# Kernel tuning notes

Measured on AMD Instinct MI355X. Metric: run time of the kernel, lower is better.

Reference implementation:

```python
import jax, jax.numpy as jnp
import numpy as np

N = 50000          # nodes
E = 1_600_000      # edges
DIN = 128          # input feature dim
HID = 32           # hidden_dim per head
HEADS = 4          # conv1 heads
G = 64             # graphs in batch
SLOPE = 0.2        # LeakyReLU negative slope (PyG GATConv default)
EPS = 1e-16


def setup_inputs() -> dict:
    key = jax.random.key(0)
    ks = jax.random.split(key, 14)
    s = 0.05
    return {
        "x": jax.random.normal(ks[0], (N, DIN), jnp.float32),
        "edge_index": jax.random.randint(ks[1], (2, E), 0, N, dtype=jnp.int64),
        "batch": jnp.sort(jax.random.randint(ks[2], (N,), 0, G, dtype=jnp.int64)),
        # conv1: GATConv(DIN, HID, heads=4, concat=True)
        "W1": jax.random.normal(ks[3], (DIN, HEADS * HID), jnp.float32) * s,
        "a_src1": jax.random.normal(ks[4], (HEADS, HID), jnp.float32) * s,
        "a_dst1": jax.random.normal(ks[5], (HEADS, HID), jnp.float32) * s,
        "b1": jax.random.normal(ks[6], (HEADS * HID,), jnp.float32) * s,
        # conv2: GATConv(4*HID, HID, heads=1)
        "W2": jax.random.normal(ks[7], (HEADS * HID, HID), jnp.float32) * s,
        "a_src2": jax.random.normal(ks[8], (1, HID), jnp.float32) * s,
        "a_dst2": jax.random.normal(ks[9], (1, HID), jnp.float32) * s,
        "b2": jax.random.normal(ks[10], (HID,), jnp.float32) * s,
        # final Linear(HID, 2)
        "Wfc": jax.random.normal(ks[11], (HID, 2), jnp.float32) * s,
        "bfc": jax.random.normal(ks[12], (2,), jnp.float32) * s,
    }


def gat_conv(x, src, dst, W, a_src, a_dst, b, heads, d):
    """PyG-style GATConv (self-loops already appended to src/dst)."""
    n = x.shape[0]
    h = (x @ W).reshape(n, heads, d)                   # [N,H,D]
    alpha_src = jnp.einsum('nhd,hd->nh', h, a_src)     # [N,H]
    alpha_dst = jnp.einsum('nhd,hd->nh', h, a_dst)     # [N,H]
    e = alpha_src[src] + alpha_dst[dst]                # [Etot,H]
    e = jnp.where(e >= 0, e, SLOPE * e)                # LeakyReLU
    # segment softmax over destination nodes
    m = jax.ops.segment_max(e, dst, num_segments=n)    # [N,H]
    e = jnp.exp(e - m[dst])
    s = jax.ops.segment_sum(e, dst, num_segments=n)    # [N,H]
    alpha = e / (s[dst] + EPS)                         # [Etot,H]
    msg = h[src] * alpha[:, :, None]                   # [Etot,H,D]
    out = jax.ops.segment_sum(msg, dst, num_segments=n)  # [N,H,D]
    return out.reshape(n, heads * d) + b               # concat heads + bias


def reference(x, edge_index, batch, W1, a_src1, a_dst1, b1,
              W2, a_src2, a_dst2, b2, Wfc, bfc):
    n = x.shape[0]
    loops = jnp.arange(n, dtype=edge_index.dtype)
    src = jnp.concatenate([edge_index[0], loops])      # add self loops
    dst = jnp.concatenate([edge_index[1], loops])

    h = gat_conv(x, src, dst, W1, a_src1, a_dst1, b1, HEADS, HID)
    h = jax.nn.elu(h)
    h = gat_conv(h, src, dst, W2, a_src2, a_dst2, b2, 1, HID)
    h = jax.nn.elu(h)

    # global mean pool over graphs
    sums = jax.ops.segment_sum(h, batch, num_segments=G)            # [G,HID]
    cnt = jax.ops.segment_sum(jnp.ones((n, 1), h.dtype), batch, num_segments=G)
    pooled = sums / jnp.maximum(cnt, 1.0)

    logits = pooled @ Wfc + bfc                                      # [G,2]
    return jax.nn.log_softmax(logits, axis=1)
```

## Files before the change

### kernel.cpp

```cpp
#include <hip/hip_runtime.h>
#include <hip/hip_fp8.h>
#include <math.h>

#define DIN   128
#define HEADS 4
#define HID   32
#define C1    (HEADS*HID)
#define NG    64
#define SLOPE 0.2f
#define EPSF  1e-16f

#define NPB   256
#define CAPQ  10240
#define CHUNK 2048

__device__ __forceinline__ unsigned int f2bf(float f) {
    unsigned int u = __float_as_uint(f);
    return (u + 0x7FFFu + ((u >> 16) & 1u)) >> 16;
}
__device__ __forceinline__ float bf_lo(unsigned int u) { return __uint_as_float(u << 16); }
__device__ __forceinline__ float bf_hi(unsigned int u) { return __uint_as_float(u & 0xFFFF0000u); }

__device__ __forceinline__ unsigned int f2fp8(float f) {
    __hip_fp8_e4m3 t(f);
    return (unsigned int)t.__x;
}
template <int SEL>
__device__ __forceinline__ float fp8tof(unsigned int u) {
#if __has_builtin(__builtin_amdgcn_cvt_f32_fp8)
    return __builtin_amdgcn_cvt_f32_fp8(u, SEL);
#else
    __hip_fp8_e4m3 t; t.__x = (unsigned char)((u >> (8 * SEL)) & 0xFFu); return (float)t;
#endif
}
typedef float f32x2 __attribute__((ext_vector_type(2)));
template <int WORD>
__device__ __forceinline__ f32x2 fp8pk(unsigned int u) {
#if __has_builtin(__builtin_amdgcn_cvt_pk_f32_fp8)
    return __builtin_amdgcn_cvt_pk_f32_fp8((int)u, WORD);
#else
    f32x2 r; r[0] = fp8tof<2 * WORD>(u); r[1] = fp8tof<2 * WORD + 1>(u); return r;
#endif
}

template <int NT>
__device__ __forceinline__ int blockScanExcl(int v, int* wsum) {
    int lane = threadIdx.x & 63, wid = threadIdx.x >> 6;
    int incl = v;
#pragma unroll
    for (int d = 1; d < 64; d <<= 1) {
        int t = __shfl_up(incl, d);
        if (lane >= d) incl += t;
    }
    if (lane == 63) wsum[wid] = incl;
    __syncthreads();
    if (threadIdx.x == 0) {
        int a = 0;
#pragma unroll
        for (int w = 0; w < NT / 64; w++) { int t = wsum[w]; wsum[w] = a; a += t; }
    }
    __syncthreads();
    return incl - v + wsum[wid];
}

__global__ void k_zero(int* gcursor, int nbuck) {
    int i = threadIdx.x;
    if (i < nbuck) gcursor[i] = 0;
}

__global__ __launch_bounds__(256) void k_binscatter(const int* __restrict__ srcs,
        const int* __restrict__ dsts, int* __restrict__ gcursor,
        unsigned int* __restrict__ stage, int E) {
    __shared__ unsigned int s_tmp[CHUNK];
    __shared__ unsigned int s_out[CHUNK];
    __shared__ int s_hist[256], s_off[256], s_base[256], s_cur[256], wsum[4];
    int tid = threadIdx.x;
    int e0 = blockIdx.x * CHUNK;
    int cnt = min(CHUNK, E - e0);
    s_hist[tid] = 0;
    __syncthreads();
    for (int i = tid; i < cnt; i += 256) {
        int sv = srcs[e0 + i];
        int dv = dsts[e0 + i];
        int b = dv >> 8;
        s_tmp[i] = ((unsigned)b << 24) | ((unsigned)(dv & (NPB - 1)) << 16) | (unsigned)sv;
        atomicAdd(&s_hist[b], 1);
    }
    __syncthreads();
    int myc = s_hist[tid];
    int excl = blockScanExcl<256>(myc, wsum);
    s_off[tid] = excl;
    s_base[tid] = myc ? atomicAdd(&gcursor[tid], myc) : 0;
    s_cur[tid] = 0;
    __syncthreads();
    for (int i = tid; i < cnt; i += 256) {
        unsigned int p = s_tmp[i];
        int b = p >> 24;
        int pos = s_off[b] + atomicAdd(&s_cur[b], 1);
        s_out[pos] = p;
    }
    __syncthreads();
    for (int i = tid; i < cnt; i += 256) {
        unsigned int p = s_out[i];
        int b = p >> 24;
        int rel = s_base[b] + (i - s_off[b]);
        if (rel < CAPQ) stage[(size_t)b * CAPQ + rel] = p & 0xFFFFFFu;
    }
}

__global__ __launch_bounds__(512) void k_bucket_build(const unsigned int* __restrict__ stage,
        const int* __restrict__ gcursor,
        int* __restrict__ rowstart, int* __restrict__ rowlen,
        int* __restrict__ esrc, int n) {
    __shared__ unsigned int s_e[CAPQ];
    __shared__ int s_cnt[256], s_offn[256], s_curn[256], wsum[8];
    __shared__ int s_eb;
    int bx = blockIdx.x, tid = threadIdx.x;
    int b = bx >> 1, hf = bx & 1;
    int cnt = min(gcursor[b], CAPQ);
    int node0 = b << 8;
    if (tid == 0) s_eb = 0;
    if (tid < 256) { s_cnt[tid] = 0; s_curn[tid] = 0; }
    __syncthreads();
    if (tid < b) atomicAdd(&s_eb, min(gcursor[tid], CAPQ));
    for (int i = tid; i < cnt; i += 512) {
        unsigned int p = stage[(size_t)b * CAPQ + i];
        s_e[i] = p;
        atomicAdd(&s_cnt[p >> 16], 1);
    }
    __syncthreads();
    int eb = s_eb;
    int myc = (tid < 256) ? s_cnt[tid] : 0;
    int excl = blockScanExcl<512>(myc, wsum);
    if (tid < 256) s_offn[tid] = excl;
    __syncthreads();
    if (tid < 128) {
        int ld = (hf << 7) + tid;
        int node = node0 + ld;
        if (node < n) { rowstart[node] = eb + s_offn[ld]; rowlen[node] = s_cnt[ld]; }
    }
    for (int i = tid; i < cnt; i += 512) {
        unsigned int p = s_e[i];
        int ld = p >> 16;
        if ((ld >> 7) == hf) {
            int pos = s_offn[ld] + atomicAdd(&s_curn[ld], 1);
            esrc[eb + pos] = (int)(p & 0xFFFFu);
        }
    }
}

#define BM1 64
#define BK1 32
__global__ __launch_bounds__(256) void k_conv1(const float* __restrict__ x, const float* __restrict__ W1,
                        const float* __restrict__ a_src, const float* __restrict__ a_dst,
                        unsigned char* __restrict__ h1f8, float* __restrict__ as1,
                        float* __restrict__ ad1, int n) {
    __shared__ float xt[BK1][BM1 + 1];
    __shared__ float ws[BK1][C1];
    int tid = threadIdx.x;
    int m0 = blockIdx.x * BM1;
    int ty = tid >> 4;
    int tx = tid & 15;
    int r0 = ty * 4;
    int c0 = tx * 8;
    float acc[4][8];
#pragma unroll
    for (int i = 0; i < 4; i++)
#pragma unroll
        for (int j = 0; j < 8; j++) acc[i][j] = 0.0f;

    for (int kb = 0; kb < DIN; kb += BK1) {
        {
            int row = tid >> 3;
            int c4  = (tid & 7) * 4;
#pragma unroll
            for (int i = 0; i < 2; i++) {
                int rr = row + i * 32;
                int g = m0 + rr;
                float4 v = make_float4(0.f, 0.f, 0.f, 0.f);
                if (g < n) v = *reinterpret_cast<const float4*>(x + (size_t)g * DIN + kb + c4);
                xt[c4 + 0][rr] = v.x; xt[c4 + 1][rr] = v.y;
                xt[c4 + 2][rr] = v.z; xt[c4 + 3][rr] = v.w;
            }
            int c4w = (tid & 31) * 4;
            int k0  = tid >> 5;
#pragma unroll
            for (int i = 0; i < 4; i++) {
                int kk = k0 + i * 8;
                *reinterpret_cast<float4*>(&ws[kk][c4w]) =
                    *reinterpret_cast<const float4*>(W1 + (size_t)(kb + kk) * C1 + c4w);
            }
        }
        __syncthreads();
#pragma unroll
        for (int kk = 0; kk < BK1; kk++) {
            float a[4], bb[8];
            *reinterpret_cast<float4*>(a)      = *reinterpret_cast<float4*>(&xt[kk][r0]);
            *reinterpret_cast<float4*>(bb)     = *reinterpret_cast<float4*>(&ws[kk][c0]);
            *reinterpret_cast<float4*>(bb + 4) = *reinterpret_cast<float4*>(&ws[kk][c0 + 4]);
#pragma unroll
            for (int i = 0; i < 4; i++)
#pragma unroll
                for (int j = 0; j < 8; j++) acc[i][j] = fmaf(a[i], bb[j], acc[i][j]);
        }
        __syncthreads();
    }
    float asv[8], adv[8];
#pragma unroll
    for (int j = 0; j < 8; j++) { asv[j] = a_src[c0 + j]; adv[j] = a_dst[c0 + j]; }
#pragma unroll
    for (int i = 0; i < 4; i++) {
        int g = m0 + r0 + i;
        float ps = 0.0f, pd = 0.0f;
#pragma unroll
        for (int j = 0; j < 8; j++) {
            ps = fmaf(acc[i][j], asv[j], ps);
            pd = fmaf(acc[i][j], adv[j], pd);
        }
        if (g < n) {
            unsigned int w0 = 0, w1 = 0;
#pragma unroll
            for (int j = 0; j < 4; j++) w0 |= f2fp8(acc[i][j]) << (8 * j);
#pragma unroll
            for (int j = 0; j < 4; j++) w1 |= f2fp8(acc[i][4 + j]) << (8 * j);
            *reinterpret_cast<uint2*>(h1f8 + (size_t)g * C1 + c0) = make_uint2(w0, w1);
        }
        ps += __shfl_xor(ps, 1); ps += __shfl_xor(ps, 2);
        pd += __shfl_xor(pd, 1); pd += __shfl_xor(pd, 2);
        if ((tx & 3) == 0 && g < n) {
            as1[g * HEADS + (tx >> 2)] = ps;
            ad1[g * HEADS + (tx >> 2)] = pd;
        }
    }
}

#define BM2 128
#define BK2 32
__global__ __launch_bounds__(256) void k_conv2(const unsigned int* __restrict__ x2u,
                        const float* __restrict__ W2,
                        const float* __restrict__ a_src, const float* __restrict__ a_dst,
                        unsigned char* __restrict__ h2f8, float* __restrict__ as2,
                        float* __restrict__ ad2, int n) {
    __shared__ float xt[BK2][BM2 + 1];
    __shared__ float ws[BK2][HID];
    int tid = threadIdx.x;
    int m0 = blockIdx.x * BM2;
    int ty = tid >> 3;
    int tx = tid & 7;
    int r0 = ty * 4;
    int c0 = tx * 4;
    float acc[4][4];
#pragma unroll
    for (int i = 0; i < 4; i++)
#pragma unroll
        for (int j = 0; j < 4; j++) acc[i][j] = 0.0f;

    for (int kb = 0; kb < C1; kb += BK2) {
        {
            int row = tid >> 3;
            int c4  = (tid & 7) * 4;
#pragma unroll
            for (int i = 0; i < 4; i++) {
                int rr = row + i * 32;
                int g = m0 + rr;
                uint2 u = make_uint2(0u, 0u);
                if (g < n) u = *reinterpret_cast<const uint2*>(x2u + (size_t)g * 64 + ((kb + c4) >> 1));
                xt[c4 + 0][rr] = bf_lo(u.x); xt[c4 + 1][rr] = bf_hi(u.x);
                xt[c4 + 2][rr] = bf_lo(u.y); xt[c4 + 3][rr] = bf_hi(u.y);
            }
            int kk = tid >> 3;
            int c4w = (tid & 7) * 4;
            *reinterpret_cast<float4*>(&ws[kk][c4w]) =
                *reinterpret_cast<const float4*>(W2 + (size_t)(kb + kk) * HID + c4w);
        }
        __syncthreads();
#pragma unroll
        for (int kk = 0; kk < BK2; kk++) {
            float a[4], bb[4];
            *reinterpret_cast<float4*>(a)  = *reinterpret_cast<float4*>(&xt[kk][r0]);
            *reinterpret_cast<float4*>(bb) = *reinterpret_cast<float4*>(&ws[kk][c0]);
#pragma unroll
            for (int i = 0; i < 4; i++)
#pragma unroll
                for (int j = 0; j < 4; j++) acc[i][j] = fmaf(a[i], bb[j], acc[i][j]);
        }
        __syncthreads();
    }
    float asv[4], adv[4];
#pragma unroll
    for (int j = 0; j < 4; j++) { asv[j] = a_src[c0 + j]; adv[j] = a_dst[c0 + j]; }
#pragma unroll
    for (int i = 0; i < 4; i++) {
        int g = m0 + r0 + i;
        float ps = 0.0f, pd = 0.0f;
#pragma unroll
        for (int j = 0; j < 4; j++) {
            ps = fmaf(acc[i][j], asv[j], ps);
            pd = fmaf(acc[i][j], adv[j], pd);
        }
        if (g < n) {
            unsigned int w = 0;
#pragma unroll
            for (int j = 0; j < 4; j++) w |= f2fp8(acc[i][j]) << (8 * j);
            *reinterpret_cast<unsigned int*>(h2f8 + (size_t)g * HID + c0) = w;
        }
        ps += __shfl_xor(ps, 1); ps += __shfl_xor(ps, 2); ps += __shfl_xor(ps, 4);
        pd += __shfl_xor(pd, 1); pd += __shfl_xor(pd, 2); pd += __shfl_xor(pd, 4);
        if (tx == 0 && g < n) { as2[g] = ps; ad2[g] = pd; }
    }
}

__global__ __launch_bounds__(256) void k_gat1(const int* __restrict__ rowstart, const int* __restrict__ rowlen,
                       const int* __restrict__ esrc,
                       const float* __restrict__ as1, const float* __restrict__ ad1,
                       const unsigned char* __restrict__ h1f8, const float* __restrict__ b1,
                       unsigned int* __restrict__ x2u, int n) {
    __shared__ float alds[4][64 * HEADS];
    __shared__ int   slds[4][64];
    const uint2* h1u2 = (const uint2*)h1f8;
    const unsigned short* h1h = (const unsigned short*)h1f8;
    int wid = threadIdx.x >> 6;
    int lane = threadIdx.x & 63;
    int nid = blockIdx.x * 4 + wid;
    bool active = nid < n;
    int start = 0, deg = 0, cnt = 1;
    if (active) { start = rowstart[nid]; deg = rowlen[nid]; cnt = deg + 1; }
    bool fast = active && (cnt <= 64);

    float adv[HEADS] = {0.f, 0.f, 0.f, 0.f};
    if (active) {
#pragma unroll
        for (int h = 0; h < HEADS; h++) adv[h] = ad1[nid * HEADS + h];
    }

    if (fast) {
        int s = nid;
        if (lane < deg) s = esrc[start + lane];
        bool act = lane < cnt;
        float4 asv = make_float4(0.f, 0.f, 0.f, 0.f);
        if (act) asv = *reinterpret_cast<const float4*>(as1 + (size_t)s * HEADS);
        float v[HEADS];
        v[0] = asv.x + adv[0]; v[1] = asv.y + adv[1];
        v[2] = asv.z + adv[2]; v[3] = asv.w + adv[3];
        float p[HEADS], sum[HEADS];
#pragma unroll
        for (int h = 0; h < HEADS; h++) {
            v[h] = (v[h] >= 0.0f) ? v[h] : SLOPE * v[h];
            p[h] = act ? __expf(v[h]) : 0.0f;
            sum[h] = p[h];
#pragma unroll
            for (int off = 32; off; off >>= 1) sum[h] += __shfl_xor(sum[h], off);
            p[h] *= 1.0f / (sum[h] + EPSF);
        }
        slds[wid][lane] = s;
        float4 pv; pv.x = p[0]; pv.y = p[1]; pv.z = p[2]; pv.w = p[3];
        *reinterpret_cast<float4*>(&alds[wid][lane * 4]) = pv;
    }
    __syncthreads();
    if (!active) return;

    if (fast) {
        int q = lane >> 4, l = lane & 15;
        int hq = l >> 2;
        float acc[8];
#pragma unroll
        for (int i = 0; i < 8; i++) acc[i] = 0.0f;
#pragma unroll 2
        for (int k = q; k < cnt; k += 4) {
            int s = slds[wid][k];
            float a = alds[wid][k * 4 + hq];
            uint2 u = h1u2[(size_t)s * 16 + l];
            f32x2 f0 = fp8pk<0>(u.x), f1 = fp8pk<1>(u.x);
            f32x2 f2 = fp8pk<0>(u.y), f3 = fp8pk<1>(u.y);
            acc[0] = fmaf(f0[0], a, acc[0]); acc[1] = fmaf(f0[1], a, acc[1]);
            acc[2] = fmaf(f1[0], a, acc[2]); acc[3] = fmaf(f1[1], a, acc[3]);
            acc[4] = fmaf(f2[0], a, acc[4]); acc[5] = fmaf(f2[1], a, acc[5]);
            acc[6] = fmaf(f3[0], a, acc[6]); acc[7] = fmaf(f3[1], a, acc[7]);
        }
#pragma unroll
        for (int i = 0; i < 8; i++) {
            acc[i] += __shfl_xor(acc[i], 16);
            acc[i] += __shfl_xor(acc[i], 32);
        }
        if (q == 0) {
            int j0 = l * 8;
            unsigned int w[4];
#pragma unroll
            for (int i = 0; i < 4; i++) {
                float o0 = acc[2 * i] + b1[j0 + 2 * i];
                float o1 = acc[2 * i + 1] + b1[j0 + 2 * i + 1];
                o0 = (o0 > 0.0f) ? o0 : expm1f(o0);
                o1 = (o1 > 0.0f) ? o1 : expm1f(o1);
                w[i] = f2bf(o0) | (f2bf(o1) << 16);
            }
            *reinterpret_cast<uint4*>(x2u + (size_t)nid * 64 + l * 4) =
                make_uint4(w[0], w[1], w[2], w[3]);
        }
    } else {
        int j = lane * 2;
        int hme = lane >> 4;
        float m[HEADS] = {-INFINITY, -INFINITY, -INFINITY, -INFINITY};
        for (int k = lane; k <= deg; k += 64) {
            int s = (k < deg) ? esrc[start + k] : nid;
#pragma unroll
            for (int h = 0; h < HEADS; h++) {
                float v = as1[s * HEADS + h] + adv[h];
                v = (v >= 0.0f) ? v : SLOPE * v;
                m[h] = fmaxf(m[h], v);
            }
        }
#pragma unroll
        for (int h = 0; h < HEADS; h++)
#pragma unroll
            for (int off = 32; off; off >>= 1) m[h] = fmaxf(m[h], __shfl_xor(m[h], off));
        float sum[HEADS] = {0.f, 0.f, 0.f, 0.f};
        for (int k = lane; k <= deg; k += 64) {
            int s = (k < deg) ? esrc[start + k] : nid;
#pragma unroll
            for (int h = 0; h < HEADS; h++) {
                float v = as1[s * HEADS + h] + adv[h];
                v = (v >= 0.0f) ? v : SLOPE * v;
                sum[h] += __expf(v - m[h]);
            }
        }
#pragma unroll
        for (int h = 0; h < HEADS; h++) {
#pragma unroll
            for (int off = 32; off; off >>= 1) sum[h] += __shfl_xor(sum[h], off);
            sum[h] = 1.0f / (sum[h] + EPSF);
        }
        float adme = adv[hme], mme = m[hme], invme = sum[hme];
        float accx = 0.0f, accy = 0.0f;
        for (int k = 0; k <= deg; k++) {
            int s = (k < deg) ? esrc[start + k] : nid;
            float v = as1[s * HEADS + hme] + adme;
            v = (v >= 0.0f) ? v : SLOPE * v;
            float alpha = __expf(v - mme) * invme;
            unsigned int u0 = h1h[(size_t)s * 64 + lane];
            accx = fmaf(fp8tof<0>(u0), alpha, accx);
            accy = fmaf(fp8tof<1>(u0), alpha, accy);
        }
        float o0 = accx + b1[j], o1 = accy + b1[j + 1];
        o0 = (o0 > 0.0f) ? o0 : expm1f(o0);
        o1 = (o1 > 0.0f) ? o1 : expm1f(o1);
        x2u[(size_t)nid * 64 + lane] = f2bf(o0) | (f2bf(o1) << 16);
    }
}

__global__ __launch_bounds__(256) void k_gat2(const int* __restrict__ rowstart, const int* __restrict__ rowlen,
                       const int* __restrict__ esrc,
                       const float* __restrict__ as2, const float* __restrict__ ad2,
                       const unsigned char* __restrict__ h2f8, const float* __restrict__ b2,
                       float* __restrict__ x3, int n) {
    __shared__ float alds[4][64];
    __shared__ int   slds[4][64];
    const unsigned short* h2h = (const unsigned short*)h2f8;
    int wid = threadIdx.x >> 6;
    int lane = threadIdx.x & 63;
    int nid = blockIdx.x * 4 + wid;
    bool active = nid < n;
    int start = 0, deg = 0, cnt = 1;
    float adv = 0.0f;
    if (active) { start = rowstart[nid]; deg = rowlen[nid]; cnt = deg + 1; adv = ad2[nid]; }
    bool fast = active && (cnt <= 64);

    if (fast) {
        int s = nid;
        if (lane < deg) s = esrc[start + lane];
        bool act = lane < cnt;
        float v = as2[s] + adv;
        v = (v >= 0.0f) ? v : SLOPE * v;
        float p = act ? __expf(v) : 0.0f;
        float sum = p;
#pragma unroll
        for (int off = 32; off; off >>= 1) sum += __shfl_xor(sum, off);
        p *= 1.0f / (sum + EPSF);
        slds[wid][lane] = s;
        alds[wid][lane] = p;
    }
    __syncthreads();
    if (!active) return;

    if (fast) {
        int q = lane >> 4, l = lane & 15;
        float acc0 = 0.0f, acc1 = 0.0f;
#pragma unroll 2
        for (int k = q; k < cnt; k += 4) {
            int s = slds[wid][k];
            float a = alds[wid][k];
            unsigned int u = h2h[(size_t)s * 16 + l];
            f32x2 f = fp8pk<0>(u);
            acc0 = fmaf(f[0], a, acc0);
            acc1 = fmaf(f[1], a, acc1);
        }
        acc0 += __shfl_xor(acc0, 16); acc0 += __shfl_xor(acc0, 32);
        acc1 += __shfl_xor(acc1, 16); acc1 += __shfl_xor(acc1, 32);
        if (q == 0) {
            int c0 = l * 2;
            float o0 = acc0 + b2[c0], o1 = acc1 + b2[c0 + 1];
            o0 = (o0 > 0.0f) ? o0 : expm1f(o0);
            o1 = (o1 > 0.0f) ? o1 : expm1f(o1);
            float2 r; r.x = o0; r.y = o1;
            *reinterpret_cast<float2*>(x3 + (size_t)nid * HID + c0) = r;
        }
    } else {
        int c = lane & 31;
        int half = lane >> 5;
        float m = -INFINITY;
        for (int k = lane; k <= deg; k += 64) {
            int s = (k < deg) ? esrc[start + k] : nid;
            float v = as2[s] + adv;
            v = (v >= 0.0f) ? v : SLOPE * v;
            m = fmaxf(m, v);
        }
#pragma unroll
        for (int off = 32; off; off >>= 1) m = fmaxf(m, __shfl_xor(m, off));
        float sum = 0.0f;
        for (int k = lane; k <= deg; k += 64) {
            int s = (k < deg) ? esrc[start + k] : nid;
            float v = as2[s] + adv;
            v = (v >= 0.0f) ? v : SLOPE * v;
            sum += __expf(v - m);
        }
#pragma unroll
        for (int off = 32; off; off >>= 1) sum += __shfl_xor(sum, off);
        float inv = 1.0f / (sum + EPSF);
        float acc = 0.0f;
        for (int k = half; k <= deg; k += 2) {
            int s = (k < deg) ? esrc[start + k] : nid;
            float v = as2[s] + adv;
            v = (v >= 0.0f) ? v : SLOPE * v;
            float alpha = __expf(v - m) * inv;
            unsigned int u = h2h[(size_t)s * 16 + (c >> 1)];
            float hv = (c & 1) ? fp8tof<1>(u) : fp8tof<0>(u);
            acc = fmaf(hv, alpha, acc);
        }
        acc += __shfl_xor(acc, 32);
        if (half == 0) {
            float o = acc + b2[c];
            o = (o > 0.0f) ? o : expm1f(o);
            x3[(size_t)nid * HID + c] = o;
        }
    }
}

__device__ __forceinline__ int lower_bound_g(const int* batch, int n, int g) {
    int lo = 0, hi = n;
    while (lo < hi) {
        int mid = (lo + hi) >> 1;
        if (batch[mid] < g) lo = mid + 1; else hi = mid;
    }
    return lo;
}

__global__ __launch_bounds__(512) void k_pool(const float* __restrict__ x3,
                       const int* __restrict__ batch,
                       float* __restrict__ pooled, int n) {
    int g = blockIdx.x;
    int start = lower_bound_g(batch, n, g);
    int end   = lower_bound_g(batch, n, g + 1);
    int c = threadIdx.x & 31;
    int row = threadIdx.x >> 5;
    float acc = 0.0f;
    for (int i = start + row; i < end; i += 16)
        acc += x3[(size_t)i * HID + c];
    __shared__ float sacc[16][HID];
    sacc[row][c] = acc;
    __syncthreads();
    if (row == 0) {
        float a = 0.0f;
#pragma unroll
        for (int p = 0; p < 16; p++) a += sacc[p][c];
        float cntf = (float)(end - start);
        pooled[g * HID + c] = a / fmaxf(cntf, 1.0f);
    }
}

__global__ void k_head(const float* __restrict__ pooled, const float* __restrict__ Wfc,
                       const float* __restrict__ bfc, float* __restrict__ out, int g_count) {
    int g = blockIdx.x * blockDim.x + threadIdx.x;
    if (g >= g_count) return;
    float l0 = bfc[0], l1 = bfc[1];
#pragma unroll
    for (int d = 0; d < HID; d++) {
        float p = pooled[g * HID + d];
        l0 = fmaf(p, Wfc[d * 2 + 0], l0);
        l1 = fmaf(p, Wfc[d * 2 + 1], l1);
    }
    float mx = fmaxf(l0, l1);
    float lse = mx + logf(expf(l0 - mx) + expf(l1 - mx));
    out[g * 2 + 0] = l0 - lse;
    out[g * 2 + 1] = l1 - lse;
}

extern "C" void kernel_launch(void* const* d_in, const int* in_sizes, int n_in,
                              void* d_out, int out_size, void* d_ws, size_t ws_size,
                              hipStream_t stream) {
    const float* x      = (const float*)d_in[0];
    const int*   ei     = (const int*)d_in[1];
    const int*   batch  = (const int*)d_in[2];
    const float* W1     = (const float*)d_in[3];
    const float* a_src1 = (const float*)d_in[4];
    const float* a_dst1 = (const float*)d_in[5];
    const float* b1     = (const float*)d_in[6];
    const float* W2     = (const float*)d_in[7];
    const float* a_src2 = (const float*)d_in[8];
    const float* a_dst2 = (const float*)d_in[9];
    const float* b2     = (const float*)d_in[10];
    const float* Wfc    = (const float*)d_in[11];
    const float* bfc    = (const float*)d_in[12];
    float* out = (float*)d_out;

    const int n = in_sizes[2];
    const int E = in_sizes[1] / 2;
    const int nbuck = (n + NPB - 1) / NPB;

    const int* srcs = ei;
    const int* dsts = ei + E;

    unsigned char* h1f8 = (unsigned char*)d_ws;
    unsigned int*  x2u  = (unsigned int*)(h1f8 + (size_t)n * C1);
    unsigned char* h2f8 = (unsigned char*)(x2u + (size_t)n * 64);
    float* x3     = (float*)(h2f8 + (size_t)n * HID);
    float* as1    = x3  + (size_t)n * HID;
    float* ad1    = as1 + (size_t)n * HEADS;
    float* as2    = ad1 + (size_t)n * HEADS;
    float* ad2    = as2 + (size_t)n;
    float* pooled = ad2 + (size_t)n;
    int* rowstart = (int*)(pooled + NG * HID);
    int* rowlen   = rowstart + n;
    int* esrc     = rowlen + n;
    int* gcursor  = esrc + E;
    unsigned int* stage = (unsigned int*)(gcursor + 256);

    k_zero<<<1, 256, 0, stream>>>(gcursor, nbuck);
    k_binscatter<<<(E + CHUNK - 1) / CHUNK, 256, 0, stream>>>(srcs, dsts, gcursor, stage, E);
    k_bucket_build<<<nbuck * 2, 512, 0, stream>>>(stage, gcursor, rowstart, rowlen, esrc, n);

    k_conv1<<<(n + BM1 - 1) / BM1, 256, 0, stream>>>(x, W1, a_src1, a_dst1, h1f8, as1, ad1, n);

    k_gat1<<<(n + 3) / 4, 256, 0, stream>>>(rowstart, rowlen, esrc, as1, ad1, h1f8, b1, x2u, n);

    k_conv2<<<(n + BM2 - 1) / BM2, 256, 0, stream>>>(x2u, W2, a_src2, a_dst2, h2f8, as2, ad2, n);

    k_gat2<<<(n + 3) / 4, 256, 0, stream>>>(rowstart, rowlen, esrc, as2, ad2, h2f8, b2, x3, n);

    k_pool<<<NG, 512, 0, stream>>>(x3, batch, pooled, n);

    k_head<<<1, 64, 0, stream>>>(pooled, Wfc, bfc, out, NG);
}
```

Measured before the change: 274.3 us.

## Drop block barriers in GAT kernels and use per-lane gather in gat1 fast path

Removes the __syncthreads barriers in k_gat1 and k_gat2, which are safe to drop because each wavefront reads only its own LDS slice, and lets out-of-range waves exit early. The gat1 fast path changes from a 4-way split over edges with cross-lane shuffle reductions to one lane per 2-channel pair, iterating over all edges with a 4-way unrolled loop. Indexing switches to 32-bit shifts, and the zeroing kernel is replaced by hipMemsetAsync. The new gather uses 2-byte loads per lane instead of 8-byte loads and walks every edge sequentially, which lengthens the per-wave loop, and the 32-bit index math assumes node offsets fit in an int.

After: 273.2 us. No clear change (-0.4%).

```diff
diff --git a/kernel.cpp b/kernel.cpp
--- a/kernel.cpp
+++ b/kernel.cpp
@@ -61,11 +61,6 @@
     }
     __syncthreads();
     return incl - v + wsum[wid];
-}
-
-__global__ void k_zero(int* gcursor, int nbuck) {
-    int i = threadIdx.x;
-    if (i < nbuck) gcursor[i] = 0;
 }
 
 __global__ __launch_bounds__(256) void k_binscatter(const int* __restrict__ srcs,
@@ -317,22 +312,22 @@
                        unsigned int* __restrict__ x2u, int n) {
     __shared__ float alds[4][64 * HEADS];
     __shared__ int   slds[4][64];
-    const uint2* h1u2 = (const uint2*)h1f8;
     const unsigned short* h1h = (const unsigned short*)h1f8;
     int wid = threadIdx.x >> 6;
     int lane = threadIdx.x & 63;
     int nid = blockIdx.x * 4 + wid;
-    bool active = nid < n;
-    int start = 0, deg = 0, cnt = 1;
-    if (active) { start = rowstart[nid]; deg = rowlen[nid]; cnt = deg + 1; }
-    bool fast = active && (cnt <= 64);
-
-    float adv[HEADS] = {0.f, 0.f, 0.f, 0.f};
-    if (active) {
-#pragma unroll
-        for (int h = 0; h < HEADS; h++) adv[h] = ad1[nid * HEADS + h];
-    }
-
+    if (nid >= n) return;
+    int start = rowstart[nid];
+    int deg   = rowlen[nid];
+    int cnt   = deg + 1;
+    bool fast = cnt <= 64;
+
+    float adv[HEADS];
+#pragma unroll
+    for (int h = 0; h < HEADS; h++) adv[h] = ad1[nid * HEADS + h];
+
+    int j = lane * 2;
+    int hme = lane >> 4;
     if (fast) {
         int s = nid;
         if (lane < deg) s = esrc[start + lane];
@@ -355,50 +350,37 @@
         slds[wid][lane] = s;
         float4 pv; pv.x = p[0]; pv.y = p[1]; pv.z = p[2]; pv.w = p[3];
         *reinterpret_cast<float4*>(&alds[wid][lane * 4]) = pv;
-    }
-    __syncthreads();
-    if (!active) return;
-
-    if (fast) {
-        int q = lane >> 4, l = lane & 15;
-        int hq = l >> 2;
-        float acc[8];
-#pragma unroll
-        for (int i = 0; i < 8; i++) acc[i] = 0.0f;
-#pragma unroll 2
-        for (int k = q; k < cnt; k += 4) {
-            int s = slds[wid][k];
-            float a = alds[wid][k * 4 + hq];
-            uint2 u = h1u2[(size_t)s * 16 + l];
-            f32x2 f0 = fp8pk<0>(u.x), f1 = fp8pk<1>(u.x);
-            f32x2 f2 = fp8pk<0>(u.y), f3 = fp8pk<1>(u.y);
-            acc[0] = fmaf(f0[0], a, acc[0]); acc[1] = fmaf(f0[1], a, acc[1]);
-            acc[2] = fmaf(f1[0], a, acc[2]); acc[3] = fmaf(f1[1], a, acc[3]);
-            acc[4] = fmaf(f2[0], a, acc[4]); acc[5] = fmaf(f2[1], a, acc[5]);
-            acc[6] = fmaf(f3[0], a, acc[6]); acc[7] = fmaf(f3[1], a, acc[7]);
-        }
-#pragma unroll
-        for (int i = 0; i < 8; i++) {
-            acc[i] += __shfl_xor(acc[i], 16);
-            acc[i] += __shfl_xor(acc[i], 32);
-        }
-        if (q == 0) {
-            int j0 = l * 8;
-            unsigned int w[4];
-#pragma unroll
-            for (int i = 0; i < 4; i++) {
-                float o0 = acc[2 * i] + b1[j0 + 2 * i];
-                float o1 = acc[2 * i + 1] + b1[j0 + 2 * i + 1];
-                o0 = (o0 > 0.0f) ? o0 : expm1f(o0);
-                o1 = (o1 > 0.0f) ? o1 : expm1f(o1);
-                w[i] = f2bf(o0) | (f2bf(o1) << 16);
-            }
-            *reinterpret_cast<uint4*>(x2u + (size_t)nid * 64 + l * 4) =
-                make_uint4(w[0], w[1], w[2], w[3]);
-        }
+
+        float accx = 0.0f, accy = 0.0f;
+        int k = 0;
+        for (; k + 3 < cnt; k += 4) {
+            int s0 = slds[wid][k],     s1 = slds[wid][k + 1];
+            int s2 = slds[wid][k + 2], s3 = slds[wid][k + 3];
+            float a0 = alds[wid][k * 4 + hme],       a1 = alds[wid][(k + 1) * 4 + hme];
+            float a2 = alds[wid][(k + 2) * 4 + hme], a3 = alds[wid][(k + 3) * 4 + hme];
+            unsigned int u0 = h1h[(s0 << 6) + lane];
+            unsigned int u1 = h1h[(s1 << 6) + lane];
+            unsigned int u2 = h1h[(s2 << 6) + lane];
+            unsigned int u3 = h1h[(s3 << 6) + lane];
+            f32x2 f0 = fp8pk<0>(u0), f1 = fp8pk<0>(u1);
+            f32x2 f2 = fp8pk<0>(u2), f3 = fp8pk<0>(u3);
+            accx = fmaf(f0[0], a0, accx); accy = fmaf(f0[1], a0, accy);
+            accx = fmaf(f1[0], a1, accx); accy = fmaf(f1[1], a1, accy);
+            accx = fmaf(f2[0], a2, accx); accy = fmaf(f2[1], a2, accy);
+            accx = fmaf(f3[0], a3, accx); accy = fmaf(f3[1], a3, accy);
+        }
+        for (; k < cnt; k++) {
+            int s0 = slds[wid][k];
+            float a0 = alds[wid][k * 4 + hme];
+            unsigned int u0 = h1h[(s0 << 6) + lane];
+            f32x2 f0 = fp8pk<0>(u0);
+            accx = fmaf(f0[0], a0, accx); accy = fmaf(f0[1], a0, accy);
+        }
+        float o0 = accx + b1[j], o1 = accy + b1[j + 1];
+        o0 = (o0 > 0.0f) ? o0 : expm1f(o0);
+        o1 = (o1 > 0.0f) ? o1 : expm1f(o1);
+        x2u[(size_t)nid * 64 + lane] = f2bf(o0) | (f2bf(o1) << 16);
     } else {
-        int j = lane * 2;
-        int hme = lane >> 4;
         float m[HEADS] = {-INFINITY, -INFINITY, -INFINITY, -INFINITY};
         for (int k = lane; k <= deg; k += 64) {
             int s = (k < deg) ? esrc[start + k] : nid;
@@ -436,9 +418,10 @@
             float v = as1[s * HEADS + hme] + adme;
             v = (v >= 0.0f) ? v : SLOPE * v;
             float alpha = __expf(v - mme) * invme;
-            unsigned int u0 = h1h[(size_t)s * 64 + lane];
-            accx = fmaf(fp8tof<0>(u0), alpha, accx);
-            accy = fmaf(fp8tof<1>(u0), alpha, accy);
+            unsigned int u0 = h1h[(s << 6) + lane];
+            f32x2 f0 = fp8pk<0>(u0);
+            accx = fmaf(f0[0], alpha, accx);
+            accy = fmaf(f0[1], alpha, accy);
         }
         float o0 = accx + b1[j], o1 = accy + b1[j + 1];
         o0 = (o0 > 0.0f) ? o0 : expm1f(o0);
@@ -458,11 +441,12 @@
     int wid = threadIdx.x >> 6;
     int lane = threadIdx.x & 63;
     int nid = blockIdx.x * 4 + wid;
-    bool active = nid < n;
-    int start = 0, deg = 0, cnt = 1;
-    float adv = 0.0f;
-    if (active) { start = rowstart[nid]; deg = rowlen[nid]; cnt = deg + 1; adv = ad2[nid]; }
-    bool fast = active && (cnt <= 64);
+    if (nid >= n) return;
+    int start = rowstart[nid];
+    int deg   = rowlen[nid];
+    int cnt   = deg + 1;
+    float adv = ad2[nid];
+    bool fast = cnt <= 64;
 
     if (fast) {
         int s = nid;
@@ -477,18 +461,14 @@
         p *= 1.0f / (sum + EPSF);
         slds[wid][lane] = s;
         alds[wid][lane] = p;
-    }
-    __syncthreads();
-    if (!active) return;
-
-    if (fast) {
+
         int q = lane >> 4, l = lane & 15;
         float acc0 = 0.0f, acc1 = 0.0f;
 #pragma unroll 2
         for (int k = q; k < cnt; k += 4) {
-            int s = slds[wid][k];
+            int sk = slds[wid][k];
             float a = alds[wid][k];
-            unsigned int u = h2h[(size_t)s * 16 + l];
+            unsigned int u = h2h[(sk << 4) + l];
             f32x2 f = fp8pk<0>(u);
             acc0 = fmaf(f[0], a, acc0);
             acc1 = fmaf(f[1], a, acc1);
@@ -531,7 +511,7 @@
             float v = as2[s] + adv;
             v = (v >= 0.0f) ? v : SLOPE * v;
             float alpha = __expf(v - m) * inv;
-            unsigned int u = h2h[(size_t)s * 16 + (c >> 1)];
+            unsigned int u = h2h[(s << 4) + (c >> 1)];
             float hv = (c & 1) ? fp8tof<1>(u) : fp8tof<0>(u);
             acc = fmaf(hv, alpha, acc);
         }
@@ -633,7 +613,7 @@
     int* gcursor  = esrc + E;
     unsigned int* stage = (unsigned int*)(gcursor + 256);
 
-    k_zero<<<1, 256, 0, stream>>>(gcursor, nbuck);
+    hipMemsetAsync(gcursor, 0, 256 * sizeof(int), stream);
     k_binscatter<<<(E + CHUNK - 1) / CHUNK, 256, 0, stream>>>(srcs, dsts, gcursor, stage, E);
     k_bucket_build<<<nbuck * 2, 512, 0, stream>>>(stage, gcursor, rowstart, rowlen, esrc, n);
 
```
